# Performance work log

Hardware: AMD Instinct MI355X
Metric: run time of the kernel (lower is better)

## Reference

```python
import jax, jax.numpy as jnp
import numpy as np

# arch = "12;cache:15,gaussian:4,identity:2,sin:1" -> segments and activations
# d_hidden = [15, 4, 2, 1], sum = 22; activations = [cache(identity), gaussian, identity, sin]
N_LAYERS = 12
D_HIDDEN = 22


def _gaussian(x):
    return jnp.exp(-x ** 2) * 2.0 - 1.0


def _act(h):
    # split into segments [15,4,2,1], apply per-segment activation, concat
    return jnp.concatenate([
        h[..., 0:15],            # cache == identity
        _gaussian(h[..., 15:19]),# gaussian
        h[..., 19:21],           # identity
        jnp.sin(h[..., 21:22]),  # sin
    ], axis=-1)


def setup_inputs() -> dict:
    key = jax.random.key(0)
    k1, k2, k3, k4 = jax.random.split(key, 4)
    N = 524288
    x = jax.random.normal(k1, (N, 4), dtype=jnp.float32)
    # lecun-style scaling (variance_scaling fan_in) approximated with scaled normal
    w_in = jax.random.normal(k2, (4, D_HIDDEN), dtype=jnp.float32) / jnp.sqrt(4.0)
    w_hidden = jax.random.normal(k3, (N_LAYERS - 1, D_HIDDEN, D_HIDDEN), dtype=jnp.float32) / jnp.sqrt(float(D_HIDDEN))
    w_out = jax.random.normal(k4, (D_HIDDEN, 3), dtype=jnp.float32) / jnp.sqrt(float(D_HIDDEN))
    return {"x": x, "w_in": w_in, "w_hidden": w_hidden, "w_out": w_out}


def reference(x, w_in, w_hidden, w_out):
    # Vectorized over pixels (batch dim N) instead of per-pixel vmap.
    features = [x]
    h = _act(jnp.einsum('ni,io->no', x, w_in))  # layer 0: [N,4]x[4,22]
    features.append(h)
    for i in range(N_LAYERS - 1):  # small fixed layer count, structurally distinct weights
        h = _act(jnp.einsum('nd,de->ne', h, w_hidden[i]))
        features.append(h)
    out = jnp.einsum('nd,do->no', h, w_out)  # [N,3] = (h,s,v)
    features.append(out)
    return (out, *features)
```

## Files before the change

### kernel.cpp

```cpp
#include <hip/hip_runtime.h>

#define NPIX 524288
#define DH 22
#define NHID 11
#define TPB 256
#define LROW 23

__device__ __forceinline__ void activate(float* h) {
#pragma unroll
    for (int j = 15; j < 19; ++j) h[j] = __expf(-h[j]*h[j]) * 2.0f - 1.0f;
    h[21] = __sinf(h[21]);
}

__device__ __forceinline__ void flush_h(float* __restrict__ gbase, const float* h,
                                        int t, float* __restrict__ lds) {
    __syncthreads();
#pragma unroll
    for (int j = 0; j < DH; ++j) lds[t * LROW + j] = h[j];
    __syncthreads();
#pragma unroll
    for (int k = 0; k < 11; ++k) {
        const int s  = t + TPB * k;
        const int pp = s / 11;
        const int r  = s - pp * 11;
        const float a = lds[pp * LROW + 2*r];
        const float b = lds[pp * LROW + 2*r + 1];
        ((float2*)gbase)[s] = make_float2(a, b);
    }
}

__global__ __launch_bounds__(256) void cppn_main(const float* __restrict__ xin,
                                                 const float* __restrict__ Win,
                                                 const float* __restrict__ Whid,
                                                 const float* __restrict__ Wout,
                                                 float* __restrict__ out) {
    __shared__ float lds[TPB * LROW];
    const int t   = threadIdx.x;
    const int blk = blockIdx.x;
    const int p   = blk * TPB + t;

    const float4 xv = ((const float4*)xin)[p];

    float h[DH];
#pragma unroll
    for (int o = 0; o < DH; ++o) {
        float a =      xv.x * Win[0*DH + o];
        a = fmaf(xv.y, Win[1*DH + o], a);
        a = fmaf(xv.z, Win[2*DH + o], a);
        a = fmaf(xv.w, Win[3*DH + o], a);
        h[o] = a;
    }
    activate(h);

    ((float4*)(out + (size_t)3 * NPIX))[p] = xv;

    float* hbase = out + (size_t)7 * NPIX + (size_t)blk * (TPB * DH);
    flush_h(hbase, h, t, lds);

    const float* Wl = Whid;
    for (int l = 0; l < NHID; ++l) {
        float hn[DH];
#pragma unroll
        for (int o = 0; o < DH; ++o) hn[o] = 0.0f;
#pragma unroll
        for (int i = 0; i < DH; ++i) {
            const float hi = h[i];
#pragma unroll
            for (int o = 0; o < DH; ++o)
                hn[o] = fmaf(hi, Wl[i*DH + o], hn[o]);
        }
        activate(hn);
#pragma unroll
        for (int o = 0; o < DH; ++o) h[o] = hn[o];
        flush_h(hbase + (size_t)(l + 1) * NPIX * DH, h, t, lds);
        Wl += DH * DH;
    }

    float o0 = 0.0f, o1 = 0.0f, o2 = 0.0f;
#pragma unroll
    for (int d = 0; d < DH; ++d) {
        o0 = fmaf(h[d], Wout[d*3 + 0], o0);
        o1 = fmaf(h[d], Wout[d*3 + 1], o1);
        o2 = fmaf(h[d], Wout[d*3 + 2], o2);
    }
    __syncthreads();
    lds[t*3 + 0] = o0; lds[t*3 + 1] = o1; lds[t*3 + 2] = o2;
    __syncthreads();
    float* g0 = out + (size_t)blk * (TPB * 3);
    float* g1 = out + (size_t)271 * NPIX + (size_t)blk * (TPB * 3);
#pragma unroll
    for (int k = 0; k < 3; ++k) {
        const int s = t + TPB * k;
        const float v = lds[s];
        g0[s] = v;
        g1[s] = v;
    }
}

extern "C" void kernel_launch(void* const* d_in, const int* in_sizes, int n_in,
                              void* d_out, int out_size, void* d_ws, size_t ws_size,
                              hipStream_t stream) {
    const float* x     = (const float*)d_in[0];
    const float* w_in  = (const float*)d_in[1];
    const float* w_hid = (const float*)d_in[2];
    const float* w_out = (const float*)d_in[3];
    float* o = (float*)d_out;

    cppn_main<<<NPIX / TPB, TPB, 0, stream>>>(x, w_in, w_hid, w_out, o);
}
```

Measured before the change: 147.3 us.

## Batch hidden-layer output stores in pairs via double LDS tile with float4 writes

Hidden activations are now staged two layers at a time in a double-sized LDS buffer, laid out contiguously per pixel, and stored to global memory as float4 with one pair of barriers per two layers instead of two barriers per layer. The final output copy is also vectorised to float4, and the x passthrough store is moved earlier. The aim is to cut barrier count and widen global stores on this store-bound kernel. The cost is doubled LDS use (about 45KB per block), which may reduce occupancy, and unpadded LDS row writes that may cause bank conflicts.

```diff
diff --git a/kernel.cpp b/kernel.cpp
--- a/kernel.cpp
+++ b/kernel.cpp
@@ -4,7 +4,8 @@
 #define DH 22
 #define NHID 11
 #define TPB 256
-#define LROW 23
+#define TILE (TPB*DH)
+#define TILE4 (TILE/4)
 
 __device__ __forceinline__ void activate(float* h) {
 #pragma unroll
@@ -12,21 +13,43 @@
     h[21] = __sinf(h[21]);
 }
 
-__device__ __forceinline__ void flush_h(float* __restrict__ gbase, const float* h,
-                                        int t, float* __restrict__ lds) {
-    __syncthreads();
+__device__ __forceinline__ void hidden_layer(float* __restrict__ h,
+                                             const float* __restrict__ W) {
+    float hn[DH];
 #pragma unroll
-    for (int j = 0; j < DH; ++j) lds[t * LROW + j] = h[j];
-    __syncthreads();
+    for (int o = 0; o < DH; ++o) hn[o] = 0.0f;
 #pragma unroll
-    for (int k = 0; k < 11; ++k) {
-        const int s  = t + TPB * k;
-        const int pp = s / 11;
-        const int r  = s - pp * 11;
-        const float a = lds[pp * LROW + 2*r];
-        const float b = lds[pp * LROW + 2*r + 1];
-        ((float2*)gbase)[s] = make_float2(a, b);
+    for (int i = 0; i < DH; ++i) {
+        const float hi = h[i];
+#pragma unroll
+        for (int o = 0; o < DH; ++o)
+            hn[o] = fmaf(hi, W[i*DH + o], hn[o]);
     }
+    activate(hn);
+#pragma unroll
+    for (int o = 0; o < DH; ++o) h[o] = hn[o];
+}
+
+__device__ __forceinline__ void write_tile(float* __restrict__ buf,
+                                           const float* __restrict__ h, int t) {
+    float2* d = (float2*)(buf + t * DH);
+#pragma unroll
+    for (int k = 0; k < 11; ++k) d[k] = make_float2(h[2*k], h[2*k+1]);
+}
+
+__device__ __forceinline__ void store_pair(float* __restrict__ g0, float* __restrict__ g1,
+                                           const float* __restrict__ lds0,
+                                           const float* __restrict__ lds1, int t) {
+    const float4* s0 = (const float4*)lds0;
+    const float4* s1 = (const float4*)lds1;
+#pragma unroll
+    for (int k = 0; k < 5; ++k) {
+        const int s = t + TPB * k;
+        ((float4*)g0)[s] = s0[s];
+        ((float4*)g1)[s] = s1[s];
+    }
+    if (t < 128) { const int s = 1280 + t;       ((float4*)g0)[s] = s0[s]; }
+    else         { const int s = 1280 + t - 128; ((float4*)g1)[s] = s1[s]; }
 }
 
 __global__ __launch_bounds__(256) void cppn_main(const float* __restrict__ xin,
@@ -34,12 +57,13 @@
                                                  const float* __restrict__ Whid,
                                                  const float* __restrict__ Wout,
                                                  float* __restrict__ out) {
-    __shared__ float lds[TPB * LROW];
+    __shared__ float lds[2 * TILE];
     const int t   = threadIdx.x;
     const int blk = blockIdx.x;
     const int p   = blk * TPB + t;
 
     const float4 xv = ((const float4*)xin)[p];
+    ((float4*)(out + (size_t)3 * NPIX))[p] = xv;
 
     float h[DH];
 #pragma unroll
@@ -52,28 +76,18 @@
     }
     activate(h);
 
-    ((float4*)(out + (size_t)3 * NPIX))[p] = xv;
+    float* hbase = out + (size_t)7 * NPIX + (size_t)blk * TILE;
+    const size_t chunk = (size_t)NPIX * DH;
 
-    float* hbase = out + (size_t)7 * NPIX + (size_t)blk * (TPB * DH);
-    flush_h(hbase, h, t, lds);
-
-    const float* Wl = Whid;
-    for (int l = 0; l < NHID; ++l) {
-        float hn[DH];
-#pragma unroll
-        for (int o = 0; o < DH; ++o) hn[o] = 0.0f;
-#pragma unroll
-        for (int i = 0; i < DH; ++i) {
-            const float hi = h[i];
-#pragma unroll
-            for (int o = 0; o < DH; ++o)
-                hn[o] = fmaf(hi, Wl[i*DH + o], hn[o]);
-        }
-        activate(hn);
-#pragma unroll
-        for (int o = 0; o < DH; ++o) h[o] = hn[o];
-        flush_h(hbase + (size_t)(l + 1) * NPIX * DH, h, t, lds);
-        Wl += DH * DH;
+    for (int i = 0; i < 6; ++i) {
+        __syncthreads();
+        write_tile(lds, h, t);
+        hidden_layer(h, Whid + (size_t)(2*i) * DH*DH);
+        write_tile(lds + TILE, h, t);
+        __syncthreads();
+        store_pair(hbase + (size_t)(2*i) * chunk,
+                   hbase + (size_t)(2*i + 1) * chunk, lds, lds + TILE, t);
+        if (i < 5) hidden_layer(h, Whid + (size_t)(2*i + 1) * DH*DH);
     }
 
     float o0 = 0.0f, o1 = 0.0f, o2 = 0.0f;
@@ -86,14 +100,10 @@
     __syncthreads();
     lds[t*3 + 0] = o0; lds[t*3 + 1] = o1; lds[t*3 + 2] = o2;
     __syncthreads();
-    float* g0 = out + (size_t)blk * (TPB * 3);
-    float* g1 = out + (size_t)271 * NPIX + (size_t)blk * (TPB * 3);
-#pragma unroll
-    for (int k = 0; k < 3; ++k) {
-        const int s = t + TPB * k;
-        const float v = lds[s];
-        g0[s] = v;
-        g1[s] = v;
+    if (t < 192) {
+        const float4 v = ((const float4*)lds)[t];
+        ((float4*)(out))[(size_t)blk * 192 + t] = v;
+        ((float4*)(out + (size_t)271 * NPIX))[(size_t)blk * 192 + t] = v;
     }
 }
 
```

After: 197.1 us. 1.34x slower.
